# Performance work log

Measured on AMD Instinct MI355X. Metric: run time of the kernel, lower is better.

## Reference

```python
import jax, jax.numpy as jnp
import numpy as np

NUM_DIM = 384
NUM_HEADS = 12
WIN = 7
L = WIN * WIN
NW = 4
B_ = 1024

def _relative_coords():
    ch, cw = np.meshgrid(np.arange(WIN), np.arange(WIN), indexing='ij')
    coords = np.stack([ch, cw]).reshape(2, -1)  # (2, L)
    rel = coords[:, :, None] - coords[:, None, :]  # (2, L, L)
    rel[0] += WIN - 1
    rel[1] += WIN - 1
    rel[0] *= 2 * WIN - 1
    return jnp.asarray(rel.sum(0), dtype=jnp.int32)  # (L, L)

def setup_inputs() -> dict:
    key = jax.random.key(0)
    k_x, k_m, k_qkv, k_pw, k_pb, k_rb = jax.random.split(key, 6)
    x = jax.random.normal(k_x, (B_, L, NUM_DIM), dtype=jnp.float32)
    mask = jax.random.bernoulli(k_m, 0.5, (NW, L, L))
    qkv_w = jax.random.normal(k_qkv, (3 * NUM_DIM, NUM_DIM), dtype=jnp.float32) * (NUM_DIM ** -0.5)
    proj_w = jax.random.normal(k_pw, (NUM_DIM, NUM_DIM), dtype=jnp.float32) * (NUM_DIM ** -0.5)
    proj_b = jax.random.normal(k_pb, (NUM_DIM,), dtype=jnp.float32) * 0.02
    rel_bias = jax.random.normal(k_rb, ((2 * WIN - 1) * (2 * WIN - 1), NUM_HEADS), dtype=jnp.float32) * 0.2
    rel_coords = _relative_coords()
    return {"x": x, "mask": mask, "qkv_w": qkv_w, "proj_w": proj_w,
            "proj_b": proj_b, "rel_bias": rel_bias, "rel_coords": rel_coords}

def reference(x, mask, qkv_w, proj_w, proj_b, rel_bias, rel_coords):
    Bt, Lx, C = x.shape
    H = NUM_HEADS
    hd = C // H
    scale = float(C) ** 0.5  # faithful: original multiplies by num_dim**0.5
    qkv = (x @ qkv_w.T).reshape(Bt, Lx, 3, H, hd).transpose(2, 0, 3, 1, 4)
    q, k, v = qkv[0], qkv[1], qkv[2]  # each (B_, H, L, hd)
    attn = jnp.einsum('bhqd,bhkd->bhqk', q, k) * scale
    bias = rel_bias[rel_coords].transpose(2, 0, 1)  # (H, L, L)
    attn = attn + bias[None]
    nw = mask.shape[0]
    attn = attn.reshape(-1, nw, H, Lx, Lx)
    attn = jnp.where(mask[None, :, None], jnp.float32(-100.0), attn)
    attn = attn.reshape(Bt, H, Lx, Lx)
    attn = jax.nn.softmax(attn, axis=-1)
    out = jnp.einsum('bhqk,bhkd->bhqd', attn, v)  # (B_, H, L, hd)
    out = out.transpose(0, 2, 1, 3).reshape(Bt, Lx, C)
    return out @ proj_w.T + proj_b
```

## Files before the change

### kernel.cpp

```cpp
#include <hip/hip_runtime.h>
#include <math.h>

#define NUM_B 1024
#define LW 49
#define CD 384
#define NH 12
#define HD 32
#define SCALE_F 19.595917942265423f

typedef unsigned short u16;
typedef unsigned int u32;
typedef __attribute__((ext_vector_type(8))) short short8;
typedef __attribute__((ext_vector_type(8))) _Float16 half8;
typedef __attribute__((ext_vector_type(4))) float floatx4;

#define ASM_VMCNT(n) asm volatile("s_waitcnt vmcnt(" #n ")" ::: "memory")
#define ASM_LGKM0()  asm volatile("s_waitcnt lgkmcnt(0)" ::: "memory")
#define BAR()        __builtin_amdgcn_s_barrier()

static __device__ __forceinline__ u16 f2bf(float f) {
    unsigned u = __float_as_uint(f);
    u += 0x7fffu + ((u >> 16) & 1u);
    return (u16)(u >> 16);
}
static __device__ __forceinline__ float bf2f(u16 s) {
    return __uint_as_float(((unsigned)s) << 16);
}
static __device__ __forceinline__ u16 f2h_bits(float f) {
    _Float16 h = (_Float16)f;
    u16 u;
    __builtin_memcpy(&u, &h, 2);
    return u;
}
static __device__ __forceinline__ void gl_lds16(const u16* g, u16* l) {
    __builtin_amdgcn_global_load_lds(
        (const __attribute__((address_space(1))) void*)g,
        (__attribute__((address_space(3))) void*)l, 16, 0, 0);
}

#define X4 4816896
#define W4 110592
#define P4 36864
#define BM4 49152
__global__ __launch_bounds__(256) void prep(const float* __restrict__ x,
                                            const float* __restrict__ qkv_w,
                                            const float* __restrict__ proj_w,
                                            const float* __restrict__ rel_bias,
                                            const int* __restrict__ rel_coords,
                                            const int* __restrict__ mask,
                                            u16* __restrict__ xbh, u16* __restrict__ xbl,
                                            u16* __restrict__ wbh, u16* __restrict__ wbl,
                                            u16* __restrict__ pfh, u16* __restrict__ pfl,
                                            float* __restrict__ bm) {
    int idx = blockIdx.x * 256 + threadIdx.x;
    if (idx < X4) {
        float4 v = ((const float4*)x)[idx];
        ushort4 h, l;
        h.x = f2bf(v.x); l.x = f2bf(v.x - bf2f(h.x));
        h.y = f2bf(v.y); l.y = f2bf(v.y - bf2f(h.y));
        h.z = f2bf(v.z); l.z = f2bf(v.z - bf2f(h.z));
        h.w = f2bf(v.w); l.w = f2bf(v.w - bf2f(h.w));
        ((ushort4*)xbh)[idx] = h;
        ((ushort4*)xbl)[idx] = l;
    } else if (idx < X4 + W4) {
        int i = idx - X4;
        float4 v = ((const float4*)qkv_w)[i];
        ushort4 h, l;
        h.x = f2bf(v.x); l.x = f2bf(v.x - bf2f(h.x));
        h.y = f2bf(v.y); l.y = f2bf(v.y - bf2f(h.y));
        h.z = f2bf(v.z); l.z = f2bf(v.z - bf2f(h.z));
        h.w = f2bf(v.w); l.w = f2bf(v.w - bf2f(h.w));
        ((ushort4*)wbh)[i] = h;
        ((ushort4*)wbl)[i] = l;
    } else if (idx < X4 + W4 + P4) {
        int i = idx - (X4 + W4);
        float4 v = ((const float4*)proj_w)[i];
        ushort4 h, l;
        h.x = f2h_bits(v.x); l.x = f2h_bits(v.x - (float)(_Float16)v.x);
        h.y = f2h_bits(v.y); l.y = f2h_bits(v.y - (float)(_Float16)v.y);
        h.z = f2h_bits(v.z); l.z = f2h_bits(v.z - (float)(_Float16)v.z);
        h.w = f2h_bits(v.w); l.w = f2h_bits(v.w - (float)(_Float16)v.w);
        ((ushort4*)pfh)[i] = h;
        ((ushort4*)pfl)[i] = l;
    } else if (idx < X4 + W4 + P4 + BM4) {
        int t = idx - (X4 + W4 + P4);
        float4 o;
        float* op = (float*)&o;
#pragma unroll
        for (int i = 0; i < 4; ++i) {
            int j = t * 4 + i;
            int e = j & 63;
            int col = (e & 3) * 16 + (e >> 2);
            int row = (j >> 6) & 63;
            int wh_ = j >> 12;
            int w = wh_ / NH;
            int h = wh_ - w * NH;
            float val = -1.0e30f;
            if (row < LW && col < LW) {
                int ij = row * LW + col;
                val = mask[w * (LW * LW) + ij] ? -1.0e4f
                                               : rel_bias[rel_coords[ij] * NH + h];
            }
            op[i] = val;
        }
        ((float4*)bm)[t] = o;
    }
}

__global__ __launch_bounds__(512) void qkv_gemm(const u16* __restrict__ Ah,
                                                const u16* __restrict__ Al,
                                                const u16* __restrict__ Wh,
                                                const u16* __restrict__ Wl,
                                                u32* __restrict__ qp,
                                                u32* __restrict__ kp,
                                                u16* __restrict__ vp) {
    __shared__ u16 As_h[2][128 * 32];
    __shared__ u16 As_l[2][128 * 32];
    __shared__ u16 Bs_h[2][128 * 32];
    __shared__ u16 Bs_l[2][128 * 32];
    const int tid = threadIdx.x;
    const int w = tid >> 6;
    const int lane = tid & 63;
    const int bid = blockIdx.x;
    const int logical = (bid & 7) * 441 + (bid >> 3);
    const int mt = logical / 9;
    const int nt = logical - mt * 9;
    const int m0 = mt * 128;
    const int n0 = nt * 128;
    const bool vblk = (nt >= 6);
    const int quad = lane >> 4;
    const int lc = lane & 15;
    const int wrow = (w >> 2) << 6;
    const int wcol = (w & 3) << 5;
    const int srow = lane >> 2;
    const int sch = (lane & 3) * 8;

    floatx4 acc[4][2];
#pragma unroll
    for (int a = 0; a < 4; ++a)
#pragma unroll
        for (int b = 0; b < 2; ++b) acc[a][b] = (floatx4){0.f, 0.f, 0.f, 0.f};

    auto stage = [&](int buf, int k0) {
        const int rb = w * 16;
        const size_t ga = (size_t)(m0 + rb + srow) * CD + k0 + sch;
        const size_t gb = (size_t)(n0 + rb + srow) * CD + k0 + sch;
        const int lof = rb * 32;
        gl_lds16(Ah + ga, As_h[buf] + lof);
        gl_lds16(Wh + gb, Bs_h[buf] + lof);
        if (!vblk) {
            gl_lds16(Al + ga, As_l[buf] + lof);
            gl_lds16(Wl + gb, Bs_l[buf] + lof);
        }
    };

    auto compute = [&](int buf) {
        if (!vblk) {
            short8 af_h[4], af_l[4], bf_h[2], bf_l[2];
#pragma unroll
            for (int t = 0; t < 4; ++t) {
                const int ar = (wrow + t * 16 + lc) * 32 + quad * 8;
                af_h[t] = *(const short8*)(As_h[buf] + ar);
                af_l[t] = *(const short8*)(As_l[buf] + ar);
            }
#pragma unroll
            for (int u = 0; u < 2; ++u) {
                const int br = (wcol + u * 16 + lc) * 32 + quad * 8;
                bf_h[u] = *(const short8*)(Bs_h[buf] + br);
                bf_l[u] = *(const short8*)(Bs_l[buf] + br);
            }
#pragma unroll
            for (int tm = 0; tm < 4; ++tm)
#pragma unroll
                for (int tn = 0; tn < 2; ++tn) {
                    acc[tm][tn] = __builtin_amdgcn_mfma_f32_16x16x32_bf16(af_h[tm], bf_h[tn], acc[tm][tn], 0, 0, 0);
                    acc[tm][tn] = __builtin_amdgcn_mfma_f32_16x16x32_bf16(af_h[tm], bf_l[tn], acc[tm][tn], 0, 0, 0);
                    acc[tm][tn] = __builtin_amdgcn_mfma_f32_16x16x32_bf16(af_l[tm], bf_h[tn], acc[tm][tn], 0, 0, 0);
                }
        } else {
            short8 af_h[4], bf_h[2];
#pragma unroll
            for (int t = 0; t < 4; ++t)
                af_h[t] = *(const short8*)(As_h[buf] + (wrow + t * 16 + lc) * 32 + quad * 8);
#pragma unroll
            for (int u = 0; u < 2; ++u)
                bf_h[u] = *(const short8*)(Bs_h[buf] + (wcol + u * 16 + lc) * 32 + quad * 8);
#pragma unroll
            for (int tm = 0; tm < 4; ++tm)
#pragma unroll
                for (int tn = 0; tn < 2; ++tn)
                    acc[tm][tn] = __builtin_amdgcn_mfma_f32_16x16x32_bf16(af_h[tm], bf_h[tn], acc[tm][tn], 0, 0, 0);
        }
    };

    stage(0, 0);
    stage(1, 32);
    if (!vblk) {
#pragma unroll
        for (int t = 0; t < 12; t += 2) {
            ASM_VMCNT(4); BAR();
            compute(0);
            ASM_LGKM0(); BAR();
            if (t + 2 < 12) { stage(0, (t + 2) * 32); ASM_VMCNT(4); }
            else            { ASM_VMCNT(0); }
            BAR();
            compute(1);
            ASM_LGKM0(); BAR();
            if (t + 2 < 12) stage(1, (t + 3) * 32);
        }
    } else {
#pragma unroll
        for (int t = 0; t < 12; t += 2) {
            ASM_VMCNT(2); BAR();
            compute(0);
            ASM_LGKM0(); BAR();
            if (t + 2 < 12) { stage(0, (t + 2) * 32); ASM_VMCNT(2); }
            else            { ASM_VMCNT(0); }
            BAR();
            compute(1);
            ASM_LGKM0(); BAR();
            if (t + 2 < 12) stage(1, (t + 3) * 32);
        }
    }

#pragma unroll
    for (int tn = 0; tn < 2; ++tn) {
        const int nst = n0 + wcol + tn * 16;
        const int t = nst / CD;
        const int rem = nst - t * CD;
        const int h = rem >> 5;
        const int db = (rem & 31) + lc;
#pragma unroll
        for (int tm = 0; tm < 4; ++tm)
#pragma unroll
            for (int r = 0; r < 4; ++r) {
                const int m = m0 + wrow + tm * 16 + quad * 4 + r;
                const int b = m / LW;
                const int l = m - b * LW;
                const size_t o = ((((size_t)b * NH + h) * LW + l) << 5) + db;
                const float vv = acc[tm][tn][r];
                if (t == 2) {
                    vp[o] = f2h_bits(vv);
                } else {
                    const unsigned bits = __float_as_uint(vv);
                    const unsigned hi_high = bits & 0xffff0000u;
                    const u16 lo = f2bf(vv - __uint_as_float(hi_high));
                    const u32 packed = hi_high | (u32)lo;
                    if (t == 0) qp[o] = packed; else kp[o] = packed;
                }
            }
    }
}

__global__ __launch_bounds__(512) void proj_gemm(const u16* __restrict__ Af,
                                                 const u16* __restrict__ Wfh,
                                                 const u16* __restrict__ Wfl,
                                                 const float* __restrict__ pb,
                                                 float* __restrict__ outF) {
    __shared__ u16 As_f[2][128 * 32];
    __shared__ u16 Bs_h[2][128 * 32];
    __shared__ u16 Bs_l[2][128 * 32];
    const int tid = threadIdx.x;
    const int w = tid >> 6;
    const int lane = tid & 63;
    const int bid = blockIdx.x;
    const int logical = (bid & 7) * 147 + (bid >> 3);
    const int mt = logical / 3;
    const int nt = logical - mt * 3;
    const int m0 = mt * 128;
    const int n0 = nt * 128;
    const int quad = lane >> 4;
    const int lc = lane & 15;
    const int wrow = (w >> 2) << 6;
    const int wcol = (w & 3) << 5;
    const int srow = lane >> 2;
    const int sch = (lane & 3) * 8;

    floatx4 acc[4][2];
#pragma unroll
    for (int a = 0; a < 4; ++a)
#pragma unroll
        for (int b = 0; b < 2; ++b) acc[a][b] = (floatx4){0.f, 0.f, 0.f, 0.f};

    auto stage = [&](int buf, int k0) {
        const int rb = w * 16;
        const size_t ga = (size_t)(m0 + rb + srow) * CD + k0 + sch;
        const size_t gb = (size_t)(n0 + rb + srow) * CD + k0 + sch;
        const int lof = rb * 32;
        gl_lds16(Af + ga, As_f[buf] + lof);
        gl_lds16(Wfh + gb, Bs_h[buf] + lof);
        gl_lds16(Wfl + gb, Bs_l[buf] + lof);
    };

    auto compute = [&](int buf) {
        half8 af[4], bh[2], bl[2];
#pragma unroll
        for (int t = 0; t < 4; ++t)
            af[t] = *(const half8*)(As_f[buf] + (wrow + t * 16 + lc) * 32 + quad * 8);
#pragma unroll
        for (int u = 0; u < 2; ++u) {
            const int br = (wcol + u * 16 + lc) * 32 + quad * 8;
            bh[u] = *(const half8*)(Bs_h[buf] + br);
            bl[u] = *(const half8*)(Bs_l[buf] + br);
        }
#pragma unroll
        for (int tm = 0; tm < 4; ++tm)
#pragma unroll
            for (int tn = 0; tn < 2; ++tn) {
                acc[tm][tn] = __builtin_amdgcn_mfma_f32_16x16x32_f16(af[tm], bh[tn], acc[tm][tn], 0, 0, 0);
                acc[tm][tn] = __builtin_amdgcn_mfma_f32_16x16x32_f16(af[tm], bl[tn], acc[tm][tn], 0, 0, 0);
            }
    };

    stage(0, 0);
    stage(1, 32);
#pragma unroll
    for (int t = 0; t < 12; t += 2) {
        ASM_VMCNT(3); BAR();
        compute(0);
        ASM_LGKM0(); BAR();
        if (t + 2 < 12) { stage(0, (t + 2) * 32); ASM_VMCNT(3); }
        else            { ASM_VMCNT(0); }
        BAR();
        compute(1);
        ASM_LGKM0(); BAR();
        if (t + 2 < 12) stage(1, (t + 3) * 32);
    }

#pragma unroll
    for (int tn = 0; tn < 2; ++tn) {
        const int n = n0 + wcol + tn * 16 + lc;
        const float bias = pb[n];
#pragma unroll
        for (int tm = 0; tm < 4; ++tm)
#pragma unroll
            for (int r = 0; r < 4; ++r) {
                const int m = m0 + wrow + tm * 16 + quad * 4 + r;
                outF[(size_t)m * CD + n] = acc[tm][tn][r] + bias;
            }
    }
}

__global__ __launch_bounds__(64) void attn_mfma(const u32* __restrict__ qp,
                                                const u32* __restrict__ kp,
                                                const u16* __restrict__ vh,
                                                const float* __restrict__ bm,
                                                u16* __restrict__ aof) {
    const int bh = blockIdx.x;
    const int b = bh / NH;
    const int h = bh - b * NH;
    const int lane = threadIdx.x;
    const int quad = lane >> 4;
    const int lc = lane & 15;
    __shared__ u16 Vt[32 * 72];
    __shared__ u16 Ps[64 * 72];

    const size_t base = (size_t)bh * (LW * HD);

    short8 aQh[4], aQl[4], bKh[4], bKl[4];
#pragma unroll
    for (int t = 0; t < 4; ++t) {
        int row = t * 16 + lc; if (row > 48) row = 48;
        const size_t o = base + (size_t)row * HD + quad * 8;
        uint4 q0 = *(const uint4*)(qp + o);
        uint4 q1 = *(const uint4*)(qp + o + 4);
        uint4 k0 = *(const uint4*)(kp + o);
        uint4 k1 = *(const uint4*)(kp + o + 4);
        unsigned qv[8] = {q0.x, q0.y, q0.z, q0.w, q1.x, q1.y, q1.z, q1.w};
        unsigned kv[8] = {k0.x, k0.y, k0.z, k0.w, k1.x, k1.y, k1.z, k1.w};
#pragma unroll
        for (int e = 0; e < 8; ++e) {
            aQh[t][e] = (short)(qv[e] >> 16);
            aQl[t][e] = (short)(qv[e] & 0xffffu);
            bKh[t][e] = (short)(kv[e] >> 16);
            bKl[t][e] = (short)(kv[e] & 0xffffu);
        }
    }
#pragma unroll
    for (int it = 0; it < 4; ++it) {
        const int idx = lane + it * 64;
        const int j = idx >> 2;
        const int jc = j > 48 ? 48 : j;
        const int ch = (idx & 3) * 8;
        short8 vv = *(const short8*)(vh + base + (size_t)jc * HD + ch);
#pragma unroll
        for (int e = 0; e < 8; ++e) Vt[(ch + e) * 72 + j] = (u16)vv[e];
    }

    floatx4 acc[4][4];
#pragma unroll
    for (int a = 0; a < 4; ++a)
#pragma unroll
        for (int c = 0; c < 4; ++c) acc[a][c] = (floatx4){0.f, 0.f, 0.f, 0.f};
#pragma unroll
    for (int tm = 0; tm < 4; ++tm)
#pragma unroll
        for (int tn = 0; tn < 4; ++tn) {
            acc[tm][tn] = __builtin_amdgcn_mfma_f32_16x16x32_bf16(aQh[tm], bKh[tn], acc[tm][tn], 0, 0, 0);
            acc[tm][tn] = __builtin_amdgcn_mfma_f32_16x16x32_bf16(aQh[tm], bKl[tn], acc[tm][tn], 0, 0, 0);
            acc[tm][tn] = __builtin_amdgcn_mfma_f32_16x16x32_bf16(aQl[tm], bKh[tn], acc[tm][tn], 0, 0, 0);
        }

    float inv_a[16];
    const float* bmp = bm + (((size_t)(b & 3) * NH + h) << 12);
#pragma unroll
    for (int tm = 0; tm < 4; ++tm)
#pragma unroll
        for (int r = 0; r < 4; ++r) {
            const int row = tm * 16 + quad * 4 + r;
            const float4 bv = *(const float4*)(bmp + row * 64 + lc * 4);
            const float s0 = fmaf(acc[tm][0][r], SCALE_F, bv.x);
            const float s1 = fmaf(acc[tm][1][r], SCALE_F, bv.y);
            const float s2 = fmaf(acc[tm][2][r], SCALE_F, bv.z);
            const float s3 = fmaf(acc[tm][3][r], SCALE_F, bv.w);
            float mx = fmaxf(fmaxf(s0, s1), fmaxf(s2, s3));
#pragma unroll
            for (int off = 1; off < 16; off <<= 1) mx = fmaxf(mx, __shfl_xor(mx, off));
            const float e0 = __expf(s0 - mx);
            const float e1 = __expf(s1 - mx);
            const float e2 = __expf(s2 - mx);
            const float e3 = __expf(s3 - mx);
            float sum = (e0 + e1) + (e2 + e3);
#pragma unroll
            for (int off = 1; off < 16; off <<= 1) sum += __shfl_xor(sum, off);
            inv_a[tm * 4 + r] = __builtin_amdgcn_rcpf(sum);
            Ps[row * 72 +  0 + lc] = f2h_bits(e0);
            Ps[row * 72 + 16 + lc] = f2h_bits(e1);
            Ps[row * 72 + 32 + lc] = f2h_bits(e2);
            Ps[row * 72 + 48 + lc] = f2h_bits(e3);
        }

    __syncthreads();

    floatx4 o[4][2];
#pragma unroll
    for (int a = 0; a < 4; ++a) { o[a][0] = (floatx4){0.f,0.f,0.f,0.f}; o[a][1] = (floatx4){0.f,0.f,0.f,0.f}; }
#pragma unroll
    for (int ks = 0; ks < 2; ++ks) {
        const half8 bV0 = *(const half8*)(Vt + (lc) * 72 + ks * 32 + quad * 8);
        const half8 bV1 = *(const half8*)(Vt + (16 + lc) * 72 + ks * 32 + quad * 8);
#pragma unroll
        for (int tm = 0; tm < 4; ++tm) {
            const half8 aP = *(const half8*)(Ps + (tm * 16 + lc) * 72 + ks * 32 + quad * 8);
            o[tm][0] = __builtin_amdgcn_mfma_f32_16x16x32_f16(aP, bV0, o[tm][0], 0, 0, 0);
            o[tm][1] = __builtin_amdgcn_mfma_f32_16x16x32_f16(aP, bV1, o[tm][1], 0, 0, 0);
        }
    }
#pragma unroll
    for (int tm = 0; tm < 4; ++tm)
#pragma unroll
        for (int r = 0; r < 4; ++r) {
            const int i = tm * 16 + quad * 4 + r;
            if (i < LW) {
                const float inv = inv_a[tm * 4 + r];
#pragma unroll
                for (int tn = 0; tn < 2; ++tn) {
                    const size_t mm = ((size_t)b * LW + i) * CD + h * HD + tn * 16 + lc;
                    aof[mm] = f2h_bits(o[tm][tn][r] * inv);
                }
            }
        }
}

extern "C" void kernel_launch(void* const* d_in, const int* in_sizes, int n_in,
                              void* d_out, int out_size, void* d_ws, size_t ws_size,
                              hipStream_t stream) {
    const float* x          = (const float*)d_in[0];
    const int*   mask       = (const int*)d_in[1];
    const float* qkv_w      = (const float*)d_in[2];
    const float* proj_w     = (const float*)d_in[3];
    const float* proj_b     = (const float*)d_in[4];
    const float* rel_bias   = (const float*)d_in[5];
    const int*   rel_coords = (const int*)d_in[6];
    float* out = (float*)d_out;

    const size_t S = (size_t)NUM_B * NH * LW * HD;
    u16* xbh = (u16*)d_ws;
    u16* xbl = xbh + S;
    u32* kp  = (u32*)(xbl + S);
    u16* vh  = (u16*)(kp + S);
    u16* wbh = vh + S;
    u16* wbl = wbh + 442368;
    u16* pfh = wbl + 442368;
    u16* pfl = pfh + 147456;
    float* bm = (float*)(pfl + 147456);
    u32* qp = (u32*)d_out;
    u16* aof = xbh;

    prep<<<dim3(19584), dim3(256), 0, stream>>>(x, qkv_w, proj_w, rel_bias, rel_coords,
                                                mask, xbh, xbl, wbh, wbl, pfh, pfl, bm);
    qkv_gemm<<<dim3(3528), dim3(512), 0, stream>>>(xbh, xbl, wbh, wbl, qp, kp, vh);
    attn_mfma<<<dim3(NUM_B * NH), dim3(64), 0, stream>>>(qp, kp, vh, bm, aof);
    proj_gemm<<<dim3(1176), dim3(512), 0, stream>>>(aof, pfh, pfl, proj_b, out);
}
```

Baseline: 377.3 us.

## Swizzle GEMM LDS tiles and split attention rows across four waves

Both GEMM kernels now stage tiles into LDS with an XOR-swizzled chunk index and read them back through a matching swizzle, to cut LDS bank conflicts on fragment loads. The attention kernel moves from one wave per (batch, head) to four waves, each owning a 16-row query tile. Each wave still loads all of K and shares V/P through LDS, so per-wave register pressure drops and parallelism rises, at the cost of redundant K loads. An unused 'sl' variable is left behind.

```diff
diff --git a/kernel.cpp b/kernel.cpp
--- a/kernel.cpp
+++ b/kernel.cpp
@@ -133,7 +133,8 @@
     const int wrow = (w >> 2) << 6;
     const int wcol = (w & 3) << 5;
     const int srow = lane >> 2;
-    const int sch = (lane & 3) * 8;
+    const int sch = (((lane & 3) ^ (srow & 3))) * 8;
+    const int sl = ((lc & 3)) * 8;
 
     floatx4 acc[4][2];
 #pragma unroll
@@ -154,20 +155,24 @@
         }
     };
 
+    auto rd = [&](const u16* base_, int row) -> short8 {
+        return *(const short8*)(base_ + row * 32 + ((quad ^ (row & 3)) * 8));
+    };
+
     auto compute = [&](int buf) {
         if (!vblk) {
             short8 af_h[4], af_l[4], bf_h[2], bf_l[2];
 #pragma unroll
             for (int t = 0; t < 4; ++t) {
-                const int ar = (wrow + t * 16 + lc) * 32 + quad * 8;
-                af_h[t] = *(const short8*)(As_h[buf] + ar);
-                af_l[t] = *(const short8*)(As_l[buf] + ar);
+                const int ar = wrow + t * 16 + lc;
+                af_h[t] = rd(As_h[buf], ar);
+                af_l[t] = rd(As_l[buf], ar);
             }
 #pragma unroll
             for (int u = 0; u < 2; ++u) {
-                const int br = (wcol + u * 16 + lc) * 32 + quad * 8;
-                bf_h[u] = *(const short8*)(Bs_h[buf] + br);
-                bf_l[u] = *(const short8*)(Bs_l[buf] + br);
+                const int br = wcol + u * 16 + lc;
+                bf_h[u] = rd(Bs_h[buf], br);
+                bf_l[u] = rd(Bs_l[buf], br);
             }
 #pragma unroll
             for (int tm = 0; tm < 4; ++tm)
@@ -181,10 +186,10 @@
             short8 af_h[4], bf_h[2];
 #pragma unroll
             for (int t = 0; t < 4; ++t)
-                af_h[t] = *(const short8*)(As_h[buf] + (wrow + t * 16 + lc) * 32 + quad * 8);
+                af_h[t] = rd(As_h[buf], wrow + t * 16 + lc);
 #pragma unroll
             for (int u = 0; u < 2; ++u)
-                bf_h[u] = *(const short8*)(Bs_h[buf] + (wcol + u * 16 + lc) * 32 + quad * 8);
+                bf_h[u] = rd(Bs_h[buf], wcol + u * 16 + lc);
 #pragma unroll
             for (int tm = 0; tm < 4; ++tm)
 #pragma unroll
@@ -222,6 +227,7 @@
             if (t + 2 < 12) stage(1, (t + 3) * 32);
         }
     }
+    (void)sl;
 
 #pragma unroll
     for (int tn = 0; tn < 2; ++tn) {
@@ -274,7 +280,7 @@
     const int wrow = (w >> 2) << 6;
     const int wcol = (w & 3) << 5;
     const int srow = lane >> 2;
-    const int sch = (lane & 3) * 8;
+    const int sch = (((lane & 3) ^ (srow & 3))) * 8;
 
     floatx4 acc[4][2];
 #pragma unroll
@@ -292,16 +298,20 @@
         gl_lds16(Wfl + gb, Bs_l[buf] + lof);
     };
 
+    auto rd = [&](const u16* base_, int row) -> half8 {
+        return *(const half8*)(base_ + row * 32 + ((quad ^ (row & 3)) * 8));
+    };
+
     auto compute = [&](int buf) {
         half8 af[4], bh[2], bl[2];
 #pragma unroll
         for (int t = 0; t < 4; ++t)
-            af[t] = *(const half8*)(As_f[buf] + (wrow + t * 16 + lc) * 32 + quad * 8);
+            af[t] = rd(As_f[buf], wrow + t * 16 + lc);
 #pragma unroll
         for (int u = 0; u < 2; ++u) {
-            const int br = (wcol + u * 16 + lc) * 32 + quad * 8;
-            bh[u] = *(const half8*)(Bs_h[buf] + br);
-            bl[u] = *(const half8*)(Bs_l[buf] + br);
+            const int br = wcol + u * 16 + lc;
+            bh[u] = rd(Bs_h[buf], br);
+            bl[u] = rd(Bs_l[buf], br);
         }
 #pragma unroll
         for (int tm = 0; tm < 4; ++tm)
@@ -341,15 +351,17 @@
     }
 }
 
-__global__ __launch_bounds__(64) void attn_mfma(const u32* __restrict__ qp,
-                                                const u32* __restrict__ kp,
-                                                const u16* __restrict__ vh,
-                                                const float* __restrict__ bm,
-                                                u16* __restrict__ aof) {
+__global__ __launch_bounds__(256) void attn_mfma(const u32* __restrict__ qp,
+                                                 const u32* __restrict__ kp,
+                                                 const u16* __restrict__ vh,
+                                                 const float* __restrict__ bm,
+                                                 u16* __restrict__ aof) {
     const int bh = blockIdx.x;
     const int b = bh / NH;
     const int h = bh - b * NH;
-    const int lane = threadIdx.x;
+    const int tid = threadIdx.x;
+    const int w = tid >> 6;
+    const int lane = tid & 63;
     const int quad = lane >> 4;
     const int lc = lane & 15;
     __shared__ u16 Vt[32 * 72];
@@ -357,28 +369,35 @@
 
     const size_t base = (size_t)bh * (LW * HD);
 
-    short8 aQh[4], aQl[4], bKh[4], bKl[4];
+    short8 aQh, aQl;
+    {
+        int row = w * 16 + lc; if (row > 48) row = 48;
+        const size_t o = base + (size_t)row * HD + quad * 8;
+        uint4 q0 = *(const uint4*)(qp + o);
+        uint4 q1 = *(const uint4*)(qp + o + 4);
+        unsigned qv[8] = {q0.x, q0.y, q0.z, q0.w, q1.x, q1.y, q1.z, q1.w};
+#pragma unroll
+        for (int e = 0; e < 8; ++e) {
+            aQh[e] = (short)(qv[e] >> 16);
+            aQl[e] = (short)(qv[e] & 0xffffu);
+        }
+    }
+    short8 bKh[4], bKl[4];
 #pragma unroll
     for (int t = 0; t < 4; ++t) {
         int row = t * 16 + lc; if (row > 48) row = 48;
         const size_t o = base + (size_t)row * HD + quad * 8;
-        uint4 q0 = *(const uint4*)(qp + o);
-        uint4 q1 = *(const uint4*)(qp + o + 4);
         uint4 k0 = *(const uint4*)(kp + o);
         uint4 k1 = *(const uint4*)(kp + o + 4);
-        unsigned qv[8] = {q0.x, q0.y, q0.z, q0.w, q1.x, q1.y, q1.z, q1.w};
         unsigned kv[8] = {k0.x, k0.y, k0.z, k0.w, k1.x, k1.y, k1.z, k1.w};
 #pragma unroll
         for (int e = 0; e < 8; ++e) {
-            aQh[t][e] = (short)(qv[e] >> 16);
-            aQl[t][e] = (short)(qv[e] & 0xffffu);
             bKh[t][e] = (short)(kv[e] >> 16);
             bKl[t][e] = (short)(kv[e] & 0xffffu);
         }
     }
-#pragma unroll
-    for (int it = 0; it < 4; ++it) {
-        const int idx = lane + it * 64;
+    {
+        const int idx = lane + w * 64;
         const int j = idx >> 2;
         const int jc = j > 48 ? 48 : j;
         const int ch = (idx & 3) * 8;
@@ -387,79 +406,65 @@
         for (int e = 0; e < 8; ++e) Vt[(ch + e) * 72 + j] = (u16)vv[e];
     }
 
-    floatx4 acc[4][4];
-#pragma unroll
-    for (int a = 0; a < 4; ++a)
-#pragma unroll
-        for (int c = 0; c < 4; ++c) acc[a][c] = (floatx4){0.f, 0.f, 0.f, 0.f};
-#pragma unroll
-    for (int tm = 0; tm < 4; ++tm)
-#pragma unroll
-        for (int tn = 0; tn < 4; ++tn) {
-            acc[tm][tn] = __builtin_amdgcn_mfma_f32_16x16x32_bf16(aQh[tm], bKh[tn], acc[tm][tn], 0, 0, 0);
-            acc[tm][tn] = __builtin_amdgcn_mfma_f32_16x16x32_bf16(aQh[tm], bKl[tn], acc[tm][tn], 0, 0, 0);
-            acc[tm][tn] = __builtin_amdgcn_mfma_f32_16x16x32_bf16(aQl[tm], bKh[tn], acc[tm][tn], 0, 0, 0);
-        }
-
-    float inv_a[16];
+    floatx4 acc[4];
+#pragma unroll
+    for (int c = 0; c < 4; ++c) acc[c] = (floatx4){0.f, 0.f, 0.f, 0.f};
+#pragma unroll
+    for (int tn = 0; tn < 4; ++tn) {
+        acc[tn] = __builtin_amdgcn_mfma_f32_16x16x32_bf16(aQh, bKh[tn], acc[tn], 0, 0, 0);
+        acc[tn] = __builtin_amdgcn_mfma_f32_16x16x32_bf16(aQh, bKl[tn], acc[tn], 0, 0, 0);
+        acc[tn] = __builtin_amdgcn_mfma_f32_16x16x32_bf16(aQl, bKh[tn], acc[tn], 0, 0, 0);
+    }
+
+    float inv_a[4];
     const float* bmp = bm + (((size_t)(b & 3) * NH + h) << 12);
 #pragma unroll
-    for (int tm = 0; tm < 4; ++tm)
-#pragma unroll
-        for (int r = 0; r < 4; ++r) {
-            const int row = tm * 16 + quad * 4 + r;
-            const float4 bv = *(const float4*)(bmp + row * 64 + lc * 4);
-            const float s0 = fmaf(acc[tm][0][r], SCALE_F, bv.x);
-            const float s1 = fmaf(acc[tm][1][r], SCALE_F, bv.y);
-            const float s2 = fmaf(acc[tm][2][r], SCALE_F, bv.z);
-            const float s3 = fmaf(acc[tm][3][r], SCALE_F, bv.w);
-            float mx = fmaxf(fmaxf(s0, s1), fmaxf(s2, s3));
-#pragma unroll
-            for (int off = 1; off < 16; off <<= 1) mx = fmaxf(mx, __shfl_xor(mx, off));
-            const float e0 = __expf(s0 - mx);
-            const float e1 = __expf(s1 - mx);
-            const float e2 = __expf(s2 - mx);
-            const float e3 = __expf(s3 - mx);
-            float sum = (e0 + e1) + (e2 + e3);
-#pragma unroll
-            for (int off = 1; off < 16; off <<= 1) sum += __shfl_xor(sum, off);
-            inv_a[tm * 4 + r] = __builtin_amdgcn_rcpf(sum);
-            Ps[row * 72 +  0 + lc] = f2h_bits(e0);
-            Ps[row * 72 + 16 + lc] = f2h_bits(e1);
-            Ps[row * 72 + 32 + lc] = f2h_bits(e2);
-            Ps[row * 72 + 48 + lc] = f2h_bits(e3);
-        }
+    for (int r = 0; r < 4; ++r) {
+        const int row = w * 16 + quad * 4 + r;
+        const float4 bv = *(const float4*)(bmp + row * 64 + lc * 4);
+        const float s0 = fmaf(acc[0][r], SCALE_F, bv.x);
+        const float s1 = fmaf(acc[1][r], SCALE_F, bv.y);
+        const float s2 = fmaf(acc[2][r], SCALE_F, bv.z);
+        const float s3 = fmaf(acc[3][r], SCALE_F, bv.w);
+        float mx = fmaxf(fmaxf(s0, s1), fmaxf(s2, s3));
+#pragma unroll
+        for (int off = 1; off < 16; off <<= 1) mx = fmaxf(mx, __shfl_xor(mx, off));
+        const float e0 = __expf(s0 - mx);
+        const float e1 = __expf(s1 - mx);
+        const float e2 = __expf(s2 - mx);
+        const float e3 = __expf(s3 - mx);
+        float sum = (e0 + e1) + (e2 + e3);
+#pragma unroll
+        for (int off = 1; off < 16; off <<= 1) sum += __shfl_xor(sum, off);
+        inv_a[r] = __builtin_amdgcn_rcpf(sum);
+        Ps[row * 72 +  0 + lc] = f2h_bits(e0);
+        Ps[row * 72 + 16 + lc] = f2h_bits(e1);
+        Ps[row * 72 + 32 + lc] = f2h_bits(e2);
+        Ps[row * 72 + 48 + lc] = f2h_bits(e3);
+    }
 
     __syncthreads();
 
-    floatx4 o[4][2];
-#pragma unroll
-    for (int a = 0; a < 4; ++a) { o[a][0] = (floatx4){0.f,0.f,0.f,0.f}; o[a][1] = (floatx4){0.f,0.f,0.f,0.f}; }
+    floatx4 o0 = (floatx4){0.f, 0.f, 0.f, 0.f};
+    floatx4 o1 = (floatx4){0.f, 0.f, 0.f, 0.f};
 #pragma unroll
     for (int ks = 0; ks < 2; ++ks) {
         const half8 bV0 = *(const half8*)(Vt + (lc) * 72 + ks * 32 + quad * 8);
         const half8 bV1 = *(const half8*)(Vt + (16 + lc) * 72 + ks * 32 + quad * 8);
-#pragma unroll
-        for (int tm = 0; tm < 4; ++tm) {
-            const half8 aP = *(const half8*)(Ps + (tm * 16 + lc) * 72 + ks * 32 + quad * 8);
-            o[tm][0] = __builtin_amdgcn_mfma_f32_16x16x32_f16(aP, bV0, o[tm][0], 0, 0, 0);
-            o[tm][1] = __builtin_amdgcn_mfma_f32_16x16x32_f16(aP, bV1, o[tm][1], 0, 0, 0);
-        }
-    }
-#pragma unroll
-    for (int tm = 0; tm < 4; ++tm)
-#pragma unroll
-        for (int r = 0; r < 4; ++r) {
-            const int i = tm * 16 + quad * 4 + r;
-            if (i < LW) {
-                const float inv = inv_a[tm * 4 + r];
-#pragma unroll
-                for (int tn = 0; tn < 2; ++tn) {
-                    const size_t mm = ((size_t)b * LW + i) * CD + h * HD + tn * 16 + lc;
-                    aof[mm] = f2h_bits(o[tm][tn][r] * inv);
-                }
-            }
-        }
+        const half8 aP = *(const half8*)(Ps + (w * 16 + lc) * 72 + ks * 32 + quad * 8);
+        o0 = __builtin_amdgcn_mfma_f32_16x16x32_f16(aP, bV0, o0, 0, 0, 0);
+        o1 = __builtin_amdgcn_mfma_f32_16x16x32_f16(aP, bV1, o1, 0, 0, 0);
+    }
+#pragma unroll
+    for (int r = 0; r < 4; ++r) {
+        const int i = w * 16 + quad * 4 + r;
+        if (i < LW) {
+            const float inv = inv_a[r];
+            const size_t mm = ((size_t)b * LW + i) * CD + h * HD + lc;
+            aof[mm] = f2h_bits(o0[r] * inv);
+            aof[mm + 16] = f2h_bits(o1[r] * inv);
+        }
+    }
 }
 
 extern "C" void kernel_launch(void* const* d_in, const int* in_sizes, int n_in,
@@ -490,6 +495,6 @@
     prep<<<dim3(19584), dim3(256), 0, stream>>>(x, qkv_w, proj_w, rel_bias, rel_coords,
                                                 mask, xbh, xbl, wbh, wbl, pfh, pfl, bm);
     qkv_gemm<<<dim3(3528), dim3(512), 0, stream>>>(xbh, xbl, wbh, wbl, qp, kp, vh);
-    attn_mfma<<<dim3(NUM_B * NH), dim3(64), 0, stream>>>(qp, kp, vh, bm, aof);
+    attn_mfma<<<dim3(NUM_B * NH), dim3(256), 0, stream>>>(qp, kp, vh, bm, aof);
     proj_gemm<<<dim3(1176), dim3(512), 0, stream>>>(aof, pfh, pfl, proj_b, out);
 }
```

Result: no change. 384.4 us (+1.9%).
